# Kernel tuning notes

Hardware: AMD Instinct MI355X
Metric: run time of the kernel (lower is better)

## Reference

```python
import jax, jax.numpy as jnp
import numpy as np

N_NODES = 100000
N_EDGES = 600000
D_IN = 128
D_HID = 128
D_OUT = 128


def setup_inputs() -> dict:
    key = jax.random.key(0)
    k = jax.random.split(key, 6)
    x = jax.random.normal(k[0], (N_NODES, D_IN), dtype=jnp.float32)
    edge_index = jax.random.randint(k[1], (2, N_EDGES), 0, N_NODES, dtype=jnp.int64)
    # GCNConv params: glorot-ish weights, zero-init biases (randn-scaled here)
    W1 = jax.random.normal(k[2], (D_IN, D_HID), dtype=jnp.float32) / np.sqrt(D_IN)
    b1 = jnp.zeros((D_HID,), dtype=jnp.float32)
    W2 = jax.random.normal(k[3], (D_HID, D_OUT), dtype=jnp.float32) / np.sqrt(D_HID)
    b2 = jnp.zeros((D_OUT,), dtype=jnp.float32)
    return {"x": x, "edge_index": edge_index, "W1": W1, "b1": b1, "W2": W2, "b2": b2}


def _gcn_conv(x, W, b, src, dst, deg_inv_sqrt, n_nodes):
    # PyG GCNConv: h = x @ W; out_i = sum_{j->i} d_j^{-1/2} d_i^{-1/2} h_j + b
    h = x @ W  # [N, Dout]
    norm = (deg_inv_sqrt[src] * deg_inv_sqrt[dst])[:, None]  # [E, 1]
    msg = h[src] * norm  # gather: [E, Dout]
    out = jax.ops.segment_sum(msg, dst, num_segments=n_nodes)  # scatter-add
    return out + b


def reference(x, edge_index, W1, b1, W2, b2):
    n = x.shape[0]
    # add self loops
    loops = jnp.arange(n, dtype=edge_index.dtype)
    src = jnp.concatenate([edge_index[0], loops])
    dst = jnp.concatenate([edge_index[1], loops])
    # symmetric normalization degrees (computed on dst, deg >= 1 due to self loops)
    deg = jax.ops.segment_sum(jnp.ones_like(dst, dtype=x.dtype), dst, num_segments=n)
    deg_inv_sqrt = jax.lax.rsqrt(deg)
    h = _gcn_conv(x, W1, b1, src, dst, deg_inv_sqrt, n)
    h = jax.nn.relu(h)  # dropout is identity in eval mode
    out = _gcn_conv(h, W2, b2, src, dst, deg_inv_sqrt, n)
    return out
```

## Files before the change

### kernel.cpp

```cpp
#include <hip/hip_runtime.h>

#define D 128

typedef __attribute__((ext_vector_type(8))) short bf16x8;
typedef __attribute__((ext_vector_type(4))) float f32x4;
typedef __attribute__((ext_vector_type(4))) unsigned u32x4;

__device__ inline unsigned short f2bf(float f) {
    unsigned u = __builtin_bit_cast(unsigned, f);
    u += 0x7FFFu + ((u >> 16) & 1u);
    return (unsigned short)(u >> 16);
}
__device__ inline float bf_lo(unsigned u) { return __builtin_bit_cast(float, u << 16); }
__device__ inline float bf_hi(unsigned u) { return __builtin_bit_cast(float, u & 0xFFFF0000u); }

__global__ void k_zero1(int* __restrict__ a, int n) {
    int i = blockIdx.x * blockDim.x + threadIdx.x;
    if (i < n) a[i] = 0;
}

__global__ void k_hist_rank(const int* __restrict__ dst, int* __restrict__ counts,
                            int* __restrict__ rank, int nE) {
    int e4 = (blockIdx.x * blockDim.x + threadIdx.x) * 4;
    if (e4 + 4 <= nE) {
        const int4 d = *reinterpret_cast<const int4*>(dst + e4);
        int4 r;
        r.x = atomicAdd(&counts[d.x], 1);
        r.y = atomicAdd(&counts[d.y], 1);
        r.z = atomicAdd(&counts[d.z], 1);
        r.w = atomicAdd(&counts[d.w], 1);
        *reinterpret_cast<int4*>(rank + e4) = r;
    } else {
        for (int e = e4; e < nE; ++e) rank[e] = atomicAdd(&counts[dst[e]], 1);
    }
}

__global__ __launch_bounds__(256) void k_scan_part(const int* __restrict__ counts,
                                                   int* __restrict__ bsum,
                                                   float* __restrict__ dis, int n) {
    const int t = threadIdx.x;
    const int base = blockIdx.x * 1024 + t * 4;
    int4 c = make_int4(0, 0, 0, 0);
    if (base + 4 <= n) {
        c = *reinterpret_cast<const int4*>(counts + base);
        float4 dv;
        dv.x = rsqrtf((float)(c.x + 1));
        dv.y = rsqrtf((float)(c.y + 1));
        dv.z = rsqrtf((float)(c.z + 1));
        dv.w = rsqrtf((float)(c.w + 1));
        *reinterpret_cast<float4*>(dis + base) = dv;
    } else if (base < n) {
        int cc[4] = {0, 0, 0, 0};
        for (int k = 0; k < 4; ++k)
            if (base + k < n) {
                cc[k] = counts[base + k];
                dis[base + k] = rsqrtf((float)(cc[k] + 1));
            }
        c.x = cc[0]; c.y = cc[1]; c.z = cc[2]; c.w = cc[3];
    }
    __shared__ int red[256];
    red[t] = c.x + c.y + c.z + c.w;
    __syncthreads();
    for (int off = 128; off > 0; off >>= 1) {
        if (t < off) red[t] += red[t + off];
        __syncthreads();
    }
    if (t == 0) bsum[blockIdx.x] = red[0];
}

__global__ __launch_bounds__(256) void k_scan_final(const int* __restrict__ counts,
                                                    const int* __restrict__ bsum,
                                                    int* __restrict__ starts, int n, int nB) {
    __shared__ int sb[128];
    __shared__ int ts[256];
    const int t = threadIdx.x;
    const int b = blockIdx.x;

    if (t < 128) sb[t] = (t < nB) ? bsum[t] : 0;
    __syncthreads();
    for (int off = 1; off < 128; off <<= 1) {
        int add = (t < 128 && t >= off) ? sb[t - off] : 0;
        __syncthreads();
        if (t < 128) sb[t] += add;
        __syncthreads();
    }
    const int block_off = (b > 0) ? sb[b - 1] : 0;

    const int base = b * 1024 + t * 4;
    int4 c = make_int4(0, 0, 0, 0);
    if (base + 4 <= n) {
        c = *reinterpret_cast<const int4*>(counts + base);
    } else if (base < n) {
        if (base + 0 < n) c.x = counts[base + 0];
        if (base + 1 < n) c.y = counts[base + 1];
        if (base + 2 < n) c.z = counts[base + 2];
    }
    const int s = c.x + c.y + c.z + c.w;
    ts[t] = s;
    __syncthreads();
    for (int off = 1; off < 256; off <<= 1) {
        int add = (t >= off) ? ts[t - off] : 0;
        __syncthreads();
        ts[t] += add;
        __syncthreads();
    }
    int excl = block_off + ts[t] - s;

    int4 w;
    w.x = excl;
    w.y = w.x + c.x;
    w.z = w.y + c.y;
    w.w = w.z + c.z;
    if (base + 4 <= n) {
        *reinterpret_cast<int4*>(starts + base) = w;
    } else if (base < n) {
        if (base + 0 < n) starts[base + 0] = w.x;
        if (base + 1 < n) starts[base + 1] = w.y;
        if (base + 2 < n) starts[base + 2] = w.z;
    }
    if (b == 0 && t == 0) starts[n] = sb[nB - 1];
}

__global__ void k_scatter_nr(const int* __restrict__ src, const int* __restrict__ dst,
                             const int* __restrict__ rank, const int* __restrict__ starts,
                             int* __restrict__ esrc, int nE) {
    int e4 = (blockIdx.x * blockDim.x + threadIdx.x) * 4;
    if (e4 + 4 <= nE) {
        const int4 s = *reinterpret_cast<const int4*>(src + e4);
        const int4 d = *reinterpret_cast<const int4*>(dst + e4);
        const int4 r = *reinterpret_cast<const int4*>(rank + e4);
        esrc[starts[d.x] + r.x] = s.x;
        esrc[starts[d.y] + r.y] = s.y;
        esrc[starts[d.z] + r.z] = s.z;
        esrc[starts[d.w] + r.w] = s.w;
    } else {
        for (int e = e4; e < nE; ++e)
            esrc[starts[dst[e]] + rank[e]] = src[e];
    }
}

template <bool IN_BF16, bool RELU>
__global__ __launch_bounds__(256, 2) void k_gemm_mfma(const void* __restrict__ Xv,
                                                      const float* __restrict__ W,
                                                      const float* __restrict__ dis,
                                                      unsigned short* __restrict__ outbf,
                                                      int n, int nst) {
    __shared__ __align__(16) unsigned short At[2][64 * 128];
    const int tid = threadIdx.x;
    const int lane = tid & 63;
    const int wv = tid >> 6;
    const int col16 = lane & 15;
    const int kgrp = lane >> 4;

    int st = blockIdx.x;
    if (st >= nst) return;

    float4 pf[8];
    bf16x8 pb[4];

    auto LOAD = [&](int t) {
#pragma unroll
        for (int c = 0; c < 4; ++c) {
            const int idx = c * 2048 + tid * 8;
            const int row = idx >> 7;
            const int col = idx & 127;
            int grow = t * 64 + row;
            if (grow >= n) grow = n - 1;
            if constexpr (IN_BF16) {
                pb[c] = *reinterpret_cast<const bf16x8*>(
                        (const unsigned short*)Xv + (size_t)grow * D + col);
            } else {
                const float4* p = reinterpret_cast<const float4*>(
                        (const float*)Xv + (size_t)grow * D + col);
                pf[2 * c] = p[0];
                pf[2 * c + 1] = p[1];
            }
        }
    };

    LOAD(st);

    bf16x8 bw[8][4];
#pragma unroll
    for (int ct = 0; ct < 8; ++ct)
#pragma unroll
        for (int kk = 0; kk < 4; ++kk)
#pragma unroll
            for (int e = 0; e < 8; ++e) {
                const int k = kk * 32 + kgrp * 8 + e;
                bw[ct][kk][e] = (short)f2bf(W[k * D + ct * 16 + col16]);
            }

    int buf = 0;
    for (;;) {
#pragma unroll
        for (int c = 0; c < 4; ++c) {
            const int idx = c * 2048 + tid * 8;
            const int row = idx >> 7;
            const int col = idx & 127;
            bf16x8 d;
            if constexpr (IN_BF16) {
                d = pb[c];
                if (RELU) {
#pragma unroll
                    for (int e = 0; e < 8; ++e)
                        d[e] = (short)((d[e] & (short)0x8000) ? 0 : d[e]);
                }
            } else {
                const float4 f0 = pf[2 * c], f1 = pf[2 * c + 1];
                float v[8] = {f0.x, f0.y, f0.z, f0.w, f1.x, f1.y, f1.z, f1.w};
#pragma unroll
                for (int e = 0; e < 8; ++e) {
                    float f = v[e];
                    if (RELU) f = fmaxf(f, 0.0f);
                    d[e] = (short)f2bf(f);
                }
            }
            const int waddr = row * 128 + (col ^ ((row & 7) << 3));
            *reinterpret_cast<bf16x8*>(&At[buf][waddr]) = d;
        }

        __syncthreads();

        bf16x8 a[4];
#pragma unroll
        for (int kk = 0; kk < 4; ++kk) {
            const int raddr = (wv * 16 + col16) * 128 +
                              ((kk * 32 + kgrp * 8) ^ ((col16 & 7) << 3));
            a[kk] = *reinterpret_cast<const bf16x8*>(&At[buf][raddr]);
        }

        const int next = st + gridDim.x;
        if (next < nst) LOAD(next);

        f32x4 acc[8];
#pragma unroll
        for (int ct = 0; ct < 8; ++ct) acc[ct] = (f32x4){0.f, 0.f, 0.f, 0.f};
#pragma unroll
        for (int kk = 0; kk < 4; ++kk)
#pragma unroll
            for (int ct = 0; ct < 8; ++ct)
                acc[ct] = __builtin_amdgcn_mfma_f32_16x16x32_bf16(a[kk], bw[ct][kk], acc[ct], 0, 0, 0);

        const int rowbase = st * 64 + wv * 16;
        float dr[4];
#pragma unroll
        for (int r = 0; r < 4; ++r) {
            const int row = rowbase + kgrp * 4 + r;
            dr[r] = (row < n) ? dis[row] : 0.0f;
        }
#pragma unroll
        for (int ct = 0; ct < 8; ++ct)
#pragma unroll
            for (int r = 0; r < 4; ++r) {
                const int row = rowbase + kgrp * 4 + r;
                if (row < n)
                    outbf[(size_t)row * D + ct * 16 + col16] = f2bf(dr[r] * acc[ct][r]);
            }

        if (next >= nst) break;
        st = next;
        buf ^= 1;
    }
}

template <bool OUT_BF16>
__global__ __launch_bounds__(256) void k_gather_agg(const unsigned short* __restrict__ hs,
                                                    const int* __restrict__ starts,
                                                    const int* __restrict__ esrc,
                                                    const float* __restrict__ dis,
                                                    const float* __restrict__ b,
                                                    void* __restrict__ outv, int n) {
    const int lane = threadIdx.x & 63;
    const int wv = threadIdx.x >> 6;
    const int grp = lane >> 4;
    const int sub = lane & 15;
    const int i = (blockIdx.x * 4 + wv) * 4 + grp;
    const bool active = (i < n);
    const int ic = active ? i : (n - 1);

    const float di = dis[ic];
    const int beg = starts[ic];
    const int end = starts[ic + 1];

    auto row16 = [&](int s) -> u32x4 {
        return *reinterpret_cast<const u32x4*>(hs + (size_t)s * D + sub * 8);
    };

    float acc[8];
    {
        const u32x4 u = row16(ic);
#pragma unroll
        for (int e = 0; e < 4; ++e) {
            acc[2 * e] = bf_lo(u[e]);
            acc[2 * e + 1] = bf_hi(u[e]);
        }
    }

#define ACCUM(u)                              \
    _Pragma("unroll") for (int e = 0; e < 4; ++e) { \
        acc[2 * e] += bf_lo((u)[e]);          \
        acc[2 * e + 1] += bf_hi((u)[e]);      \
    }

    int j = beg;
    while (j < end) {
        const int cnt = min(end - j, 16);
        const int myedge = (sub < cnt) ? esrc[j + sub] : 0;
        int k = 0;
        for (; k + 4 <= cnt; k += 4) {
            const int s0 = __shfl(myedge, (grp << 4) | (k + 0));
            const int s1 = __shfl(myedge, (grp << 4) | (k + 1));
            const int s2 = __shfl(myedge, (grp << 4) | (k + 2));
            const int s3 = __shfl(myedge, (grp << 4) | (k + 3));
            const u32x4 u0 = row16(s0);
            const u32x4 u1 = row16(s1);
            const u32x4 u2 = row16(s2);
            const u32x4 u3 = row16(s3);
            ACCUM(u0) ACCUM(u1) ACCUM(u2) ACCUM(u3)
        }
        for (; k < cnt; ++k) {
            const int s0 = __shfl(myedge, (grp << 4) | k);
            const u32x4 u0 = row16(s0);
            ACCUM(u0)
        }
        j += 16;
    }
#undef ACCUM

    if (!active) return;

    const float4 bv0 = reinterpret_cast<const float4*>(b)[sub * 2 + 0];
    const float4 bv1 = reinterpret_cast<const float4*>(b)[sub * 2 + 1];
    float o[8];
    o[0] = di * acc[0] + bv0.x; o[1] = di * acc[1] + bv0.y;
    o[2] = di * acc[2] + bv0.z; o[3] = di * acc[3] + bv0.w;
    o[4] = di * acc[4] + bv1.x; o[5] = di * acc[5] + bv1.y;
    o[6] = di * acc[6] + bv1.z; o[7] = di * acc[7] + bv1.w;

    if constexpr (OUT_BF16) {
        u32x4 w;
#pragma unroll
        for (int e = 0; e < 4; ++e)
            w[e] = (unsigned)f2bf(o[2 * e]) | ((unsigned)f2bf(o[2 * e + 1]) << 16);
        *reinterpret_cast<u32x4*>((unsigned short*)outv + (size_t)i * D + sub * 8) = w;
    } else {
        float4* op = reinterpret_cast<float4*>((float*)outv + (size_t)i * D + sub * 8);
        op[0] = make_float4(o[0], o[1], o[2], o[3]);
        op[1] = make_float4(o[4], o[5], o[6], o[7]);
    }
}

extern "C" void kernel_launch(void* const* d_in, const int* in_sizes, int n_in,
                              void* d_out, int out_size, void* d_ws, size_t ws_size,
                              hipStream_t stream) {
    const float* x  = (const float*)d_in[0];
    const int*   ei = (const int*)d_in[1];
    const float* W1 = (const float*)d_in[2];
    const float* b1 = (const float*)d_in[3];
    const float* W2 = (const float*)d_in[4];
    const float* b2 = (const float*)d_in[5];
    float* out = (float*)d_out;

    const int n  = in_sizes[0] / D;
    const int nE = in_sizes[1] / 2;
    const int* src = ei;
    const int* dst = ei + nE;

    char* ws = (char*)d_ws;
    float*          dis    = (float*)(ws);
    int*            counts = (int*)(ws + (1ull  << 19));
    int*            starts = (int*)(ws + (2ull  << 19));
    int*            esrc   = (int*)(ws + (4ull  << 19));
    int*            bsum   = (int*)(ws + (6ull  << 20));
    unsigned short* hs_bf  = (unsigned short*)(ws + (8ull  << 20));
    int*            rank   = (int*)(ws + (34ull << 20));
    unsigned short* agg_bf = (unsigned short*)(ws + (40ull << 20));

    const int B = 256;
    const int gn = (n + B - 1) / B;
    const int ge4 = (nE + B * 4 - 1) / (B * 4);
    const int nB = (n + 1023) / 1024;

    k_zero1<<<gn, B, 0, stream>>>(counts, n);
    k_hist_rank<<<ge4, B, 0, stream>>>(dst, counts, rank, nE);
    k_scan_part<<<nB, B, 0, stream>>>(counts, bsum, dis, n);
    k_scan_final<<<nB, B, 0, stream>>>(counts, bsum, starts, n, nB);
    k_scatter_nr<<<ge4, B, 0, stream>>>(src, dst, rank, starts, esrc, nE);

    const int nst = (n + 63) / 64;
    const int gemm_blocks = 512;
    const int agg_grid = (n + 15) / 16;

    k_gemm_mfma<false, false><<<gemm_blocks, B, 0, stream>>>(x, W1, dis, hs_bf, n, nst);
    k_gather_agg<true><<<agg_grid, B, 0, stream>>>(hs_bf, starts, esrc, dis, b1, agg_bf, n);

    k_gemm_mfma<true, true><<<gemm_blocks, B, 0, stream>>>(agg_bf, W2, dis, hs_bf, n, nst);
    k_gather_agg<false><<<agg_grid, B, 0, stream>>>(hs_bf, starts, esrc, dis, b2, out, n);
}
```

Measured before the change: 172.4 us.

## Prepack bf16 weight fragments, use one tile per block, vectorize GEMM output stores

Adds a small kernel that converts W1 and W2 to bf16 once, already laid out as MFMA B-fragments. The GEMM blocks then load their weights with vector reads instead of doing strided fp32 loads and conversions in every block. The persistent 512-block loop with double-buffered LDS and prefetch is replaced by one 64-row tile per block, launched over all tiles. The MFMA operands are swapped so each lane holds four contiguous output columns of one node, which allows packed 8-byte stores instead of scattered 2-byte stores. The trade-off is two extra small launches and the loss of load/compute overlap across tiles within a block.

```diff
diff --git a/kernel.cpp b/kernel.cpp
--- a/kernel.cpp
+++ b/kernel.cpp
@@ -139,128 +139,120 @@
     }
 }
 
+__global__ __launch_bounds__(256) void k_pack_w(const float* __restrict__ W,
+                                                unsigned short* __restrict__ wp) {
+    const int t = blockIdx.x * blockDim.x + threadIdx.x;
+    const int lane = t & 63;
+    const int frag = t >> 6;
+    const int ct = frag >> 2;
+    const int kk = frag & 3;
+    const int col16 = lane & 15;
+    const int kgrp = lane >> 4;
+    bf16x8 d;
+#pragma unroll
+    for (int e = 0; e < 8; ++e)
+        d[e] = (short)f2bf(W[(kk * 32 + kgrp * 8 + e) * D + ct * 16 + col16]);
+    *reinterpret_cast<bf16x8*>(wp + (size_t)t * 8) = d;
+}
+
 template <bool IN_BF16, bool RELU>
 __global__ __launch_bounds__(256, 2) void k_gemm_mfma(const void* __restrict__ Xv,
-                                                      const float* __restrict__ W,
+                                                      const unsigned short* __restrict__ wp,
                                                       const float* __restrict__ dis,
                                                       unsigned short* __restrict__ outbf,
-                                                      int n, int nst) {
-    __shared__ __align__(16) unsigned short At[2][64 * 128];
+                                                      int n) {
+    __shared__ __align__(16) unsigned short At[64 * 128];
     const int tid = threadIdx.x;
     const int lane = tid & 63;
     const int wv = tid >> 6;
     const int col16 = lane & 15;
     const int kgrp = lane >> 4;
-
-    int st = blockIdx.x;
-    if (st >= nst) return;
+    const int st = blockIdx.x;
 
     float4 pf[8];
     bf16x8 pb[4];
-
-    auto LOAD = [&](int t) {
-#pragma unroll
-        for (int c = 0; c < 4; ++c) {
-            const int idx = c * 2048 + tid * 8;
-            const int row = idx >> 7;
-            const int col = idx & 127;
-            int grow = t * 64 + row;
-            if (grow >= n) grow = n - 1;
-            if constexpr (IN_BF16) {
-                pb[c] = *reinterpret_cast<const bf16x8*>(
-                        (const unsigned short*)Xv + (size_t)grow * D + col);
-            } else {
-                const float4* p = reinterpret_cast<const float4*>(
-                        (const float*)Xv + (size_t)grow * D + col);
-                pf[2 * c] = p[0];
-                pf[2 * c + 1] = p[1];
+#pragma unroll
+    for (int c = 0; c < 4; ++c) {
+        const int idx = c * 2048 + tid * 8;
+        const int row = idx >> 7;
+        const int col = idx & 127;
+        int grow = st * 64 + row;
+        if (grow >= n) grow = n - 1;
+        if constexpr (IN_BF16) {
+            pb[c] = *reinterpret_cast<const bf16x8*>(
+                    (const unsigned short*)Xv + (size_t)grow * D + col);
+        } else {
+            const float4* p = reinterpret_cast<const float4*>(
+                    (const float*)Xv + (size_t)grow * D + col);
+            pf[2 * c] = p[0];
+            pf[2 * c + 1] = p[1];
+        }
+    }
+
+    bf16x8 bw[8][4];
+#pragma unroll
+    for (int ct = 0; ct < 8; ++ct)
+#pragma unroll
+        for (int kk = 0; kk < 4; ++kk)
+            bw[ct][kk] = *reinterpret_cast<const bf16x8*>(
+                    wp + (size_t)((ct * 4 + kk) * 64 + lane) * 8);
+
+#pragma unroll
+    for (int c = 0; c < 4; ++c) {
+        const int idx = c * 2048 + tid * 8;
+        const int row = idx >> 7;
+        const int col = idx & 127;
+        bf16x8 d;
+        if constexpr (IN_BF16) {
+            d = pb[c];
+            if (RELU) {
+#pragma unroll
+                for (int e = 0; e < 8; ++e)
+                    d[e] = (short)((d[e] & (short)0x8000) ? 0 : d[e]);
             }
-        }
-    };
-
-    LOAD(st);
-
-    bf16x8 bw[8][4];
-#pragma unroll
-    for (int ct = 0; ct < 8; ++ct)
-#pragma unroll
-        for (int kk = 0; kk < 4; ++kk)
+        } else {
+            const float4 f0 = pf[2 * c], f1 = pf[2 * c + 1];
+            float v[8] = {f0.x, f0.y, f0.z, f0.w, f1.x, f1.y, f1.z, f1.w};
 #pragma unroll
             for (int e = 0; e < 8; ++e) {
-                const int k = kk * 32 + kgrp * 8 + e;
-                bw[ct][kk][e] = (short)f2bf(W[k * D + ct * 16 + col16]);
+                float f = v[e];
+                if (RELU) f = fmaxf(f, 0.0f);
+                d[e] = (short)f2bf(f);
             }
-
-    int buf = 0;
-    for (;;) {
-#pragma unroll
-        for (int c = 0; c < 4; ++c) {
-            const int idx = c * 2048 + tid * 8;
-            const int row = idx >> 7;
-            const int col = idx & 127;
-            bf16x8 d;
-            if constexpr (IN_BF16) {
-                d = pb[c];
-                if (RELU) {
-#pragma unroll
-                    for (int e = 0; e < 8; ++e)
-                        d[e] = (short)((d[e] & (short)0x8000) ? 0 : d[e]);
-                }
-            } else {
-                const float4 f0 = pf[2 * c], f1 = pf[2 * c + 1];
-                float v[8] = {f0.x, f0.y, f0.z, f0.w, f1.x, f1.y, f1.z, f1.w};
-#pragma unroll
-                for (int e = 0; e < 8; ++e) {
-                    float f = v[e];
-                    if (RELU) f = fmaxf(f, 0.0f);
-                    d[e] = (short)f2bf(f);
-                }
-            }
-            const int waddr = row * 128 + (col ^ ((row & 7) << 3));
-            *reinterpret_cast<bf16x8*>(&At[buf][waddr]) = d;
-        }
-
-        __syncthreads();
-
-        bf16x8 a[4];
-#pragma unroll
-        for (int kk = 0; kk < 4; ++kk) {
-            const int raddr = (wv * 16 + col16) * 128 +
-                              ((kk * 32 + kgrp * 8) ^ ((col16 & 7) << 3));
-            a[kk] = *reinterpret_cast<const bf16x8*>(&At[buf][raddr]);
-        }
-
-        const int next = st + gridDim.x;
-        if (next < nst) LOAD(next);
-
-        f32x4 acc[8];
-#pragma unroll
-        for (int ct = 0; ct < 8; ++ct) acc[ct] = (f32x4){0.f, 0.f, 0.f, 0.f};
-#pragma unroll
-        for (int kk = 0; kk < 4; ++kk)
-#pragma unroll
-            for (int ct = 0; ct < 8; ++ct)
-                acc[ct] = __builtin_amdgcn_mfma_f32_16x16x32_bf16(a[kk], bw[ct][kk], acc[ct], 0, 0, 0);
-
-        const int rowbase = st * 64 + wv * 16;
-        float dr[4];
-#pragma unroll
-        for (int r = 0; r < 4; ++r) {
-            const int row = rowbase + kgrp * 4 + r;
-            dr[r] = (row < n) ? dis[row] : 0.0f;
-        }
+        }
+        const int waddr = row * 128 + (col ^ ((row & 7) << 3));
+        *reinterpret_cast<bf16x8*>(&At[waddr]) = d;
+    }
+    __syncthreads();
+
+    bf16x8 a[4];
+#pragma unroll
+    for (int kk = 0; kk < 4; ++kk) {
+        const int raddr = (wv * 16 + col16) * 128 +
+                          ((kk * 32 + kgrp * 8) ^ ((col16 & 7) << 3));
+        a[kk] = *reinterpret_cast<const bf16x8*>(&At[raddr]);
+    }
+
+    f32x4 acc[8];
+#pragma unroll
+    for (int ct = 0; ct < 8; ++ct) acc[ct] = (f32x4){0.f, 0.f, 0.f, 0.f};
+#pragma unroll
+    for (int kk = 0; kk < 4; ++kk)
 #pragma unroll
         for (int ct = 0; ct < 8; ++ct)
-#pragma unroll
-            for (int r = 0; r < 4; ++r) {
-                const int row = rowbase + kgrp * 4 + r;
-                if (row < n)
-                    outbf[(size_t)row * D + ct * 16 + col16] = f2bf(dr[r] * acc[ct][r]);
-            }
-
-        if (next >= nst) break;
-        st = next;
-        buf ^= 1;
+            acc[ct] = __builtin_amdgcn_mfma_f32_16x16x32_bf16(bw[ct][kk], a[kk], acc[ct], 0, 0, 0);
+
+    const int node = st * 64 + wv * 16 + col16;
+    if (node < n) {
+        const float dn = dis[node];
+        unsigned short* op = outbf + (size_t)node * D + kgrp * 4;
+#pragma unroll
+        for (int ct = 0; ct < 8; ++ct) {
+            uint2 w;
+            w.x = (unsigned)f2bf(dn * acc[ct][0]) | ((unsigned)f2bf(dn * acc[ct][1]) << 16);
+            w.y = (unsigned)f2bf(dn * acc[ct][2]) | ((unsigned)f2bf(dn * acc[ct][3]) << 16);
+            *reinterpret_cast<uint2*>(op + ct * 16) = w;
+        }
     }
 }
 
@@ -375,12 +367,17 @@
     int*            bsum   = (int*)(ws + (6ull  << 20));
     unsigned short* hs_bf  = (unsigned short*)(ws + (8ull  << 20));
     int*            rank   = (int*)(ws + (34ull << 20));
+    unsigned short* wp1    = (unsigned short*)(ws + (37ull << 20));
+    unsigned short* wp2    = (unsigned short*)(ws + (37ull << 20) + (1ull << 15));
     unsigned short* agg_bf = (unsigned short*)(ws + (40ull << 20));
 
     const int B = 256;
     const int gn = (n + B - 1) / B;
     const int ge4 = (nE + B * 4 - 1) / (B * 4);
     const int nB = (n + 1023) / 1024;
+
+    k_pack_w<<<8, B, 0, stream>>>(W1, wp1);
+    k_pack_w<<<8, B, 0, stream>>>(W2, wp2);
 
     k_zero1<<<gn, B, 0, stream>>>(counts, n);
     k_hist_rank<<<ge4, B, 0, stream>>>(dst, counts, rank, nE);
@@ -389,12 +386,11 @@
     k_scatter_nr<<<ge4, B, 0, stream>>>(src, dst, rank, starts, esrc, nE);
 
     const int nst = (n + 63) / 64;
-    const int gemm_blocks = 512;
     const int agg_grid = (n + 15) / 16;
 
-    k_gemm_mfma<false, false><<<gemm_blocks, B, 0, stream>>>(x, W1, dis, hs_bf, n, nst);
+    k_gemm_mfma<false, false><<<nst, B, 0, stream>>>(x, wp1, dis, hs_bf, n);
     k_gather_agg<true><<<agg_grid, B, 0, stream>>>(hs_bf, starts, esrc, dis, b1, agg_bf, n);
 
-    k_gemm_mfma<true, true><<<gemm_blocks, B, 0, stream>>>(agg_bf, W2, dis, hs_bf, n, nst);
+    k_gemm_mfma<true, true><<<nst, B, 0, stream>>>(agg_bf, wp2, dis, hs_bf, n);
     k_gather_agg<false><<<agg_grid, B, 0, stream>>>(hs_bf, starts, esrc, dis, b2, out, n);
 }
```

New measurement: 158.0 us. 8.4% less time.
